# Optimization experiments

Hardware: AMD Instinct MI355X
Metric: run time of the kernel (lower is better)

Reference implementation:

```python
import jax, jax.numpy as jnp
import numpy as np

B, T, I, H, O = 64, 512, 256, 1024, 10

def setup_inputs() -> dict:
    key = jax.random.key(0)
    ks = jax.random.split(key, 7)
    s_x = 1.0 / np.sqrt(I)
    s_h = 1.0 / np.sqrt(H)
    return {
        "x": jax.random.normal(ks[0], (B, T, I), dtype=jnp.float32),
        "Wx": jax.random.uniform(ks[1], (4, I, H), jnp.float32, -s_x, s_x),
        "bx": jax.random.uniform(ks[2], (4, H), jnp.float32, -s_x, s_x),
        "Wh": jax.random.uniform(ks[3], (4, H, H), jnp.float32, -s_h, s_h),
        "bh": jax.random.uniform(ks[4], (4, H), jnp.float32, -s_h, s_h),
        "Wp": jax.random.uniform(ks[5], (H, O), jnp.float32, -s_h, s_h),
        "bp": jax.random.uniform(ks[6], (O,), jnp.float32, -s_h, s_h),
    }

def reference(x, Wx, bx, Wh, bh, Wp, bp):
    # Gate order along axis 0: g (tanh), i, f, o (sigmoid).
    batch, seq, _ = x.shape
    hid = Wh.shape[-1]
    # Precompute all input-side gate projections: [T, 4, B, H]
    gx_all = jnp.einsum('bti,kih->tkbh', x, Wx) + bx[None, :, None, :]

    def step(carry, gx_t):
        h, c = carry
        z = gx_t + jnp.einsum('bh,kho->kbo', h, Wh) + bh[:, None, :]  # [4,B,H]
        g = jnp.tanh(z[0])
        i = jax.nn.sigmoid(z[1])
        f = jax.nn.sigmoid(z[2])
        o = jax.nn.sigmoid(z[3])
        c = g * i + c * f
        h = jnp.tanh(c) * o
        return (h, c), None

    h0 = jnp.zeros((batch, hid), dtype=x.dtype)
    c0 = jnp.zeros((batch, hid), dtype=x.dtype)
    (h, _), _ = jax.lax.scan(step, (h0, c0), gx_all)
    p = h @ Wp + bp
    return jax.nn.softmax(p, axis=1)
```

## Files before the change

### kernel.cpp

```cpp
#include <hip/hip_runtime.h>
#include <cstdint>
#include <cstddef>

#define B_  64
#define T_  512
#define I_  256
#define H_  1024
#define O_  10
#define ZST 68
#define ZPW (64 * ZST)
#define ZBUF (4 * ZPW)
#define LDS_ALLOC 139264

typedef __attribute__((ext_vector_type(4))) float f32x4;
typedef __attribute__((ext_vector_type(8))) short s16x8;
typedef unsigned long long u64;

__device__ inline unsigned short f2bf(float f) {
    unsigned int u = __float_as_uint(f);
    u += 0x7fffu + ((u >> 16) & 1u);
    return (unsigned short)(u >> 16);
}
__device__ inline float bf2f(unsigned short h) {
    return __uint_as_float(((unsigned int)h) << 16);
}
__device__ inline float fsig(float x)  { return 1.0f / (1.0f + __expf(-x)); }
__device__ inline float ftanh(float x) { return 1.0f - 2.0f / (1.0f + __expf(2.0f * x)); }

#define ALD32(p)    __hip_atomic_load((p), __ATOMIC_RELAXED, __HIP_MEMORY_SCOPE_AGENT)
#define AST32(p, v) __hip_atomic_store((p), (v), __ATOMIC_RELAXED, __HIP_MEMORY_SCOPE_AGENT)
#define ALD64(p)    __hip_atomic_load((p), __ATOMIC_RELAXED, __HIP_MEMORY_SCOPE_AGENT)
#define AST64(p, v) __hip_atomic_store((p), (v), __ATOMIC_RELAXED, __HIP_MEMORY_SCOPE_AGENT)

#define PIN_A(x) asm volatile("" : "+a"(x))

__global__ __launch_bounds__(256) void cast_xT_kernel(const float* __restrict__ x,
                                                      unsigned short* __restrict__ xb) {
    int idx = blockIdx.x * 256 + threadIdx.x;
    int ic4 = idx & 63, rest = idx >> 6;
    int t = rest & 511, b = rest >> 9;
    float4 v = ((const float4*)x)[((size_t)(b * T_ + t)) * 64 + ic4];
    ((ushort4*)xb)[((size_t)(t * B_ + b)) * 64 + ic4] =
        make_ushort4(f2bf(v.x), f2bf(v.y), f2bf(v.z), f2bf(v.w));
}

__global__ __launch_bounds__(256) void pack_wh_kernel(const float* __restrict__ Wh,
                                                      uint4* __restrict__ whp) {
    int e = blockIdx.x * 256 + threadIdx.x;
    int lane = e & 63, nt = (e >> 6) & 3, kt = (e >> 8) & 31, nb = e >> 13;
    int q = (lane & 15) >> 2, cc = lane & 3;
    int hh = nb * 16 + nt * 4 + cc;
    int k0 = kt * 32 + (lane >> 4) * 8;
    const float* src = Wh + (size_t)q * (H_ * H_) + (size_t)k0 * H_ + hh;
    unsigned short u[8];
#pragma unroll
    for (int j = 0; j < 8; ++j) u[j] = f2bf(src[(size_t)j * H_]);
    uint4 out;
    out.x = (unsigned)u[0] | ((unsigned)u[1] << 16);
    out.y = (unsigned)u[2] | ((unsigned)u[3] << 16);
    out.z = (unsigned)u[4] | ((unsigned)u[5] << 16);
    out.w = (unsigned)u[6] | ((unsigned)u[7] << 16);
    whp[e] = out;
}

__global__ __launch_bounds__(256) void pack_wx_kernel(const float* __restrict__ Wx,
                                                      uint4* __restrict__ wxp) {
    int e = blockIdx.x * 256 + threadIdx.x;
    int lane = e & 63, nt = (e >> 6) & 3, kt = (e >> 8) & 7, nb = e >> 11;
    int q = (lane & 15) >> 2, cc = lane & 3;
    int hh = nb * 16 + nt * 4 + cc;
    int i0 = kt * 32 + (lane >> 4) * 8;
    const float* src = Wx + (size_t)q * (I_ * H_) + (size_t)i0 * H_ + hh;
    unsigned short u[8];
#pragma unroll
    for (int j = 0; j < 8; ++j) u[j] = f2bf(src[(size_t)j * H_]);
    uint4 out;
    out.x = (unsigned)u[0] | ((unsigned)u[1] << 16);
    out.y = (unsigned)u[2] | ((unsigned)u[3] << 16);
    out.z = (unsigned)u[4] | ((unsigned)u[5] << 16);
    out.w = (unsigned)u[6] | ((unsigned)u[7] << 16);
    wxp[e] = out;
}

__global__ __launch_bounds__(256, 1) void lstm_kernel(const unsigned short* __restrict__ xb,
                                                      const uint4* __restrict__ whp,
                                                      const uint4* __restrict__ wxp,
                                                      const float* __restrict__ bx,
                                                      const float* __restrict__ bh,
                                                      const float* __restrict__ Wp,
                                                      const float* __restrict__ bp,
                                                      unsigned short* __restrict__ hbuf,
                                                      unsigned int* __restrict__ flags,
                                                      float* __restrict__ out) {
    extern __shared__ float zpart[];
    int tid = threadIdx.x, lane = tid & 63, w = tid >> 6;
    int nb = blockIdx.x;
    unsigned int* done = flags + 768;

    if (nb >= 64) {
        float a = 1.0f + (float)tid * 0.001f;
        const float bm = 1.0000001f, cm = 0.9999999f;
        while (ALD32(done) == 0u) {
#pragma unroll
            for (int i = 0; i < 512; ++i) a = __builtin_fmaf(a, bm, cm);
        }
        if (__float_as_uint(a) == 0xDEADBEEFu) AST32(&flags[200], 1u);
        return;
    }

    int ma = lane & 15, quad = lane >> 4;

    const s16x8* whpp = (const s16x8*)whp;
    const s16x8* wxpp = (const s16x8*)wxp;
    s16x8 whf[4][8], wxf[4][2];
#pragma unroll
    for (int nt = 0; nt < 4; ++nt) {
#pragma unroll
        for (int k = 0; k < 8; ++k)
            whf[nt][k] = whpp[nb * 8192 + (w * 8 + k) * 256 + nt * 64 + lane];
#pragma unroll
        for (int k = 0; k < 2; ++k)
            wxf[nt][k] = wxpp[nb * 2048 + (w * 2 + k) * 256 + nt * 64 + lane];
    }
#pragma unroll
    for (int nt = 0; nt < 4; ++nt) {
#pragma unroll
        for (int k = 0; k < 8; ++k) PIN_A(whf[nt][k]);
#pragma unroll
        for (int k = 0; k < 2; ++k) PIN_A(wxf[nt][k]);
    }

    int gb = tid >> 2, wq = tid & 3;
    float bias[4][4];
#pragma unroll
    for (int g = 0; g < 4; ++g)
#pragma unroll
        for (int i = 0; i < 4; ++i) {
            int n = g * H_ + nb * 16 + wq * 4 + i;
            bias[g][i] = bx[n] + bh[n];
        }

    u64* hbase = (u64*)hbuf;

    AST64(&hbase[nb * 256 + tid], 0ull);
    asm volatile("s_waitcnt vmcnt(0)" ::: "memory");
    if (lane == 0) AST32(&flags[nb * 4 + w], 1u);

    float cst[4] = {0.f, 0.f, 0.f, 0.f};

    for (int t = 0; t < T_; ++t) {
        s16x8 Ax[4][2];
#pragma unroll
        for (int mt = 0; mt < 4; ++mt) {
            const unsigned short* xrow =
                xb + ((size_t)t * B_ + mt * 16 + ma) * I_ + w * 64 + quad * 8;
            Ax[mt][0] = *(const s16x8*)xrow;
            Ax[mt][1] = *(const s16x8*)(xrow + 32);
        }
        unsigned probe = ALD32(&flags[w * 64 + lane]);
        __builtin_amdgcn_sched_barrier(0);

        f32x4 acc[4][4] = {};
#pragma unroll
        for (int mt = 0; mt < 4; ++mt)
#pragma unroll
            for (int kx = 0; kx < 2; ++kx)
#pragma unroll
                for (int nt = 0; nt < 4; ++nt)
                    acc[mt][nt] = __builtin_amdgcn_mfma_f32_16x16x32_bf16(Ax[mt][kx], wxf[nt][kx],
                                                                          acc[mt][nt], 0, 0, 0);
        __builtin_amdgcn_sched_barrier(0);

        {
            unsigned tgt = (unsigned)(t + 1);
            if (__ballot(probe < tgt) != 0ull) {
                for (;;) {
                    unsigned v = ALD32(&flags[w * 64 + lane]);
                    if (__ballot(v < tgt) == 0ull) break;
                    __builtin_amdgcn_s_sleep(1);
                }
            }
        }

        const u64* hp = hbase + (size_t)(t & 3) * 16384;
        u64*       hn = hbase + (size_t)((t + 1) & 3) * 16384;

        u64 Ah[4][16];
#pragma unroll
        for (int mt = 0; mt < 4; ++mt) {
            int row = mt * 16 + ma;
#pragma unroll
            for (int kl = 0; kl < 8; ++kl) {
                const u64* p = hp + ((size_t)((w * 8 + kl) * 2 + (quad >> 1))) * 256
                               + (size_t)row * 4 + (quad & 1) * 2;
                Ah[mt][kl * 2]     = ALD64(p);
                Ah[mt][kl * 2 + 1] = ALD64(p + 1);
            }
        }

#pragma unroll
        for (int mt = 0; mt < 4; ++mt) {
#pragma unroll
            for (int kl = 0; kl < 8; ++kl) {
                union { u64 q[2]; s16x8 v; } au;
                au.q[0] = Ah[mt][kl * 2];
                au.q[1] = Ah[mt][kl * 2 + 1];
#pragma unroll
                for (int nt = 0; nt < 4; ++nt)
                    acc[mt][nt] = __builtin_amdgcn_mfma_f32_16x16x32_bf16(au.v, whf[nt][kl],
                                                                          acc[mt][nt], 0, 0, 0);
            }
        }

        float* zb = zpart + (size_t)(t & 1) * ZBUF;
        float* zp = zb + w * ZPW;
#pragma unroll
        for (int mt = 0; mt < 4; ++mt)
#pragma unroll
            for (int nt = 0; nt < 4; ++nt)
#pragma unroll
                for (int r = 0; r < 4; ++r)
                    zp[(mt * 16 + quad * 4 + r) * ZST + nt * 16 + ma] = acc[mt][nt][r];
        __syncthreads();

        float zs[4][4];
#pragma unroll
        for (int g = 0; g < 4; ++g) {
            float4 s = make_float4(0.f, 0.f, 0.f, 0.f);
#pragma unroll
            for (int p = 0; p < 4; ++p) {
                float4 v = *(const float4*)(zb + p * ZPW + gb * ZST + wq * 16 + g * 4);
                s.x += v.x; s.y += v.y; s.z += v.z; s.w += v.w;
            }
            zs[g][0] = s.x; zs[g][1] = s.y; zs[g][2] = s.z; zs[g][3] = s.w;
        }
        unsigned short hh[4];
#pragma unroll
        for (int i = 0; i < 4; ++i) {
            float g  = ftanh(zs[0][i] + bias[0][i]);
            float ii = fsig (zs[1][i] + bias[1][i]);
            float ff = fsig (zs[2][i] + bias[2][i]);
            float oo = fsig (zs[3][i] + bias[3][i]);
            float c  = g * ii + cst[i] * ff;
            cst[i] = c;
            hh[i] = f2bf(ftanh(c) * oo);
        }
        u64 hv = (u64)hh[0] | ((u64)hh[1] << 16) | ((u64)hh[2] << 32) | ((u64)hh[3] << 48);
        AST64(&hn[nb * 256 + tid], hv);

        asm volatile("s_waitcnt vmcnt(0)" ::: "memory");
        if (lane == 0) AST32(&flags[nb * 4 + w], (unsigned)(t + 2));
    }

    {
        unsigned tgt = (unsigned)(T_ + 1);
        for (;;) {
            unsigned v = ALD32(&flags[w * 64 + lane]);
            if (__ballot(v < tgt) == 0ull) break;
            __builtin_amdgcn_s_sleep(1);
        }
    }
    __syncthreads();
    if (nb == 0 && tid == 0) AST32(done, 1u);

    int b = nb;
    union { u64 q; unsigned short s[4]; } hu;
    hu.q = ALD64(&hbase[(tid >> 2) * 256 + b * 4 + (tid & 3)]);
    int j0 = (tid >> 2) * 16 + (tid & 3) * 4;
    float pacc[O_];
#pragma unroll
    for (int o = 0; o < O_; ++o) pacc[o] = 0.f;
#pragma unroll
    for (int j = 0; j < 4; ++j) {
        float hvv = bf2f(hu.s[j]);
        const float* wr = Wp + (size_t)(j0 + j) * O_;
#pragma unroll
        for (int o = 0; o < O_; ++o) pacc[o] += hvv * wr[o];
    }
    float* red = zpart;
#pragma unroll
    for (int o = 0; o < O_; ++o) red[tid * O_ + o] = pacc[o];
    __syncthreads();
    for (int s2 = 128; s2 > 0; s2 >>= 1) {
        if (tid < s2) {
#pragma unroll
            for (int o = 0; o < O_; ++o) red[tid * O_ + o] += red[(tid + s2) * O_ + o];
        }
        __syncthreads();
    }
    if (tid == 0) {
        float p[O_];
        for (int o = 0; o < O_; ++o) p[o] = red[o] + bp[o];
        float mx = p[0];
        for (int o = 1; o < O_; ++o) mx = fmaxf(mx, p[o]);
        float e[O_], sum = 0.f;
        for (int o = 0; o < O_; ++o) { e[o] = __expf(p[o] - mx); sum += e[o]; }
        float inv = 1.f / sum;
        for (int o = 0; o < O_; ++o) out[b * O_ + o] = e[o] * inv;
    }
}

extern "C" void kernel_launch(void* const* d_in, const int* in_sizes, int n_in,
                              void* d_out, int out_size, void* d_ws, size_t ws_size,
                              hipStream_t stream) {
    (void)in_sizes; (void)n_in; (void)out_size; (void)ws_size;
    const float* x  = (const float*)d_in[0];
    const float* Wx = (const float*)d_in[1];
    const float* bx = (const float*)d_in[2];
    const float* Wh = (const float*)d_in[3];
    const float* bh = (const float*)d_in[4];
    const float* Wp = (const float*)d_in[5];
    const float* bp = (const float*)d_in[6];

    const size_t xbB  = (size_t)T_ * B_ * I_ * 2;
    const size_t whpB = (size_t)4 * H_ * H_ * 2;
    const size_t wxpB = (size_t)4 * I_ * H_ * 2;
    const size_t hB   = (size_t)4 * B_ * H_ * 2;

    char* ws = (char*)d_ws;
    unsigned short* xb    = (unsigned short*)ws;
    uint4*          whp   = (uint4*)(ws + xbB);
    uint4*          wxp   = (uint4*)(ws + xbB + whpB);
    unsigned short* hbuf  = (unsigned short*)(ws + xbB + whpB + wxpB);
    unsigned int*   flags = (unsigned int*)(ws + xbB + whpB + wxpB + hB);

    static bool attr_set = false;
    if (!attr_set) {
        (void)hipFuncSetAttribute((const void*)lstm_kernel,
                                  hipFuncAttributeMaxDynamicSharedMemorySize, LDS_ALLOC);
        attr_set = true;
    }

    hipError_t e0 = hipMemsetAsync(flags, 0, 4096, stream);
    (void)e0;
    cast_xT_kernel<<<8192, 256, 0, stream>>>(x, xb);
    pack_wh_kernel<<<2048, 256, 0, stream>>>(Wh, whp);
    pack_wx_kernel<<< 512, 256, 0, stream>>>(Wx, wxp);
    lstm_kernel<<<64 + 192, 256, LDS_ALLOC, stream>>>(xb, whp, wxp, bx, bh, Wp, bp, hbuf, flags,
                                                      (float*)d_out);
}
```

Baseline: 3.726 ms.

## Replace per-step flag barrier with NaN-sentinel polling on hidden state buffer

Removes the per-timestep flag publish and flag spin-wait between workgroups. Consumers now read the h buffer directly and re-poll any 64-bit chunk that still holds a bf16 NaN sentinel. Producers reset the slot two steps ahead to the sentinel, and a new kernel pre-fills the 4-slot ring. This drops a vmcnt drain and a flag round trip from the critical path each step. The cost is repeated polling of many h words, and correctness now relies on no real h value equalling the sentinel and on ordering of the relaxed stores.

Result: slower. 5.015 ms (+34.6%).

```diff
diff --git a/kernel.cpp b/kernel.cpp
--- a/kernel.cpp
+++ b/kernel.cpp
@@ -16,6 +16,8 @@
 typedef __attribute__((ext_vector_type(8))) short s16x8;
 typedef unsigned long long u64;
 
+#define SENT 0x7FC07FC07FC07FC0ull
+
 __device__ inline unsigned short f2bf(float f) {
     unsigned int u = __float_as_uint(f);
     u += 0x7fffu + ((u >> 16) & 1u);
@@ -80,6 +82,11 @@
     out.z = (unsigned)u[4] | ((unsigned)u[5] << 16);
     out.w = (unsigned)u[6] | ((unsigned)u[7] << 16);
     wxp[e] = out;
+}
+
+__global__ __launch_bounds__(256) void fill_sent_kernel(u64* __restrict__ hb) {
+    int i = blockIdx.x * 256 + threadIdx.x;
+    hb[i] = SENT;
 }
 
 __global__ __launch_bounds__(256, 1) void lstm_kernel(const unsigned short* __restrict__ xb,
@@ -143,8 +150,6 @@
     u64* hbase = (u64*)hbuf;
 
     AST64(&hbase[nb * 256 + tid], 0ull);
-    asm volatile("s_waitcnt vmcnt(0)" ::: "memory");
-    if (lane == 0) AST32(&flags[nb * 4 + w], 1u);
 
     float cst[4] = {0.f, 0.f, 0.f, 0.f};
 
@@ -156,30 +161,6 @@
                 xb + ((size_t)t * B_ + mt * 16 + ma) * I_ + w * 64 + quad * 8;
             Ax[mt][0] = *(const s16x8*)xrow;
             Ax[mt][1] = *(const s16x8*)(xrow + 32);
-        }
-        unsigned probe = ALD32(&flags[w * 64 + lane]);
-        __builtin_amdgcn_sched_barrier(0);
-
-        f32x4 acc[4][4] = {};
-#pragma unroll
-        for (int mt = 0; mt < 4; ++mt)
-#pragma unroll
-            for (int kx = 0; kx < 2; ++kx)
-#pragma unroll
-                for (int nt = 0; nt < 4; ++nt)
-                    acc[mt][nt] = __builtin_amdgcn_mfma_f32_16x16x32_bf16(Ax[mt][kx], wxf[nt][kx],
-                                                                          acc[mt][nt], 0, 0, 0);
-        __builtin_amdgcn_sched_barrier(0);
-
-        {
-            unsigned tgt = (unsigned)(t + 1);
-            if (__ballot(probe < tgt) != 0ull) {
-                for (;;) {
-                    unsigned v = ALD32(&flags[w * 64 + lane]);
-                    if (__ballot(v < tgt) == 0ull) break;
-                    __builtin_amdgcn_s_sleep(1);
-                }
-            }
         }
 
         const u64* hp = hbase + (size_t)(t & 3) * 16384;
@@ -197,6 +178,51 @@
                 Ah[mt][kl * 2 + 1] = ALD64(p + 1);
             }
         }
+        __builtin_amdgcn_sched_barrier(0);
+
+        f32x4 acc[4][4] = {};
+#pragma unroll
+        for (int mt = 0; mt < 4; ++mt)
+#pragma unroll
+            for (int nt = 0; nt < 4; ++nt) PIN_A(acc[mt][nt]);
+#pragma unroll
+        for (int mt = 0; mt < 4; ++mt)
+#pragma unroll
+            for (int kx = 0; kx < 2; ++kx)
+#pragma unroll
+                for (int nt = 0; nt < 4; ++nt)
+                    acc[mt][nt] = __builtin_amdgcn_mfma_f32_16x16x32_bf16(Ax[mt][kx], wxf[nt][kx],
+                                                                          acc[mt][nt], 0, 0, 0);
+        __builtin_amdgcn_sched_barrier(0);
+
+        {
+            bool any = false;
+#pragma unroll
+            for (int mt = 0; mt < 4; ++mt)
+#pragma unroll
+                for (int k = 0; k < 16; ++k) any |= (Ah[mt][k] == SENT);
+            while (__ballot(any) != 0ull) {
+                __builtin_amdgcn_s_sleep(1);
+#pragma unroll
+                for (int mt = 0; mt < 4; ++mt) {
+                    int row = mt * 16 + ma;
+#pragma unroll
+                    for (int kl = 0; kl < 8; ++kl) {
+                        if (Ah[mt][kl * 2] == SENT || Ah[mt][kl * 2 + 1] == SENT) {
+                            const u64* p = hp + ((size_t)((w * 8 + kl) * 2 + (quad >> 1))) * 256
+                                           + (size_t)row * 4 + (quad & 1) * 2;
+                            Ah[mt][kl * 2]     = ALD64(p);
+                            Ah[mt][kl * 2 + 1] = ALD64(p + 1);
+                        }
+                    }
+                }
+                any = false;
+#pragma unroll
+                for (int mt = 0; mt < 4; ++mt)
+#pragma unroll
+                    for (int k = 0; k < 16; ++k) any |= (Ah[mt][k] == SENT);
+            }
+        }
 
 #pragma unroll
         for (int mt = 0; mt < 4; ++mt) {
@@ -210,6 +236,11 @@
                     acc[mt][nt] = __builtin_amdgcn_mfma_f32_16x16x32_bf16(au.v, whf[nt][kl],
                                                                           acc[mt][nt], 0, 0, 0);
             }
+        }
+
+        {
+            u64* hf = hbase + (size_t)((t + 2) & 3) * 16384;
+            AST64(&hf[nb * 256 + tid], SENT);
         }
 
         float* zb = zpart + (size_t)(t & 1) * ZBUF;
@@ -247,11 +278,10 @@
         }
         u64 hv = (u64)hh[0] | ((u64)hh[1] << 16) | ((u64)hh[2] << 32) | ((u64)hh[3] << 48);
         AST64(&hn[nb * 256 + tid], hv);
-
-        asm volatile("s_waitcnt vmcnt(0)" ::: "memory");
-        if (lane == 0) AST32(&flags[nb * 4 + w], (unsigned)(t + 2));
-    }
-
+    }
+
+    asm volatile("s_waitcnt vmcnt(0)" ::: "memory");
+    if (lane == 0) AST32(&flags[nb * 4 + w], (unsigned)(T_ + 1));
     {
         unsigned tgt = (unsigned)(T_ + 1);
         for (;;) {
@@ -336,6 +366,7 @@
     cast_xT_kernel<<<8192, 256, 0, stream>>>(x, xb);
     pack_wh_kernel<<<2048, 256, 0, stream>>>(Wh, whp);
     pack_wx_kernel<<< 512, 256, 0, stream>>>(Wx, wxp);
+    fill_sent_kernel<<<256, 256, 0, stream>>>((u64*)hbuf);
     lstm_kernel<<<64 + 192, 256, LDS_ALLOC, stream>>>(xb, whp, wxp, bx, bh, Wp, bp, hbuf, flags,
                                                       (float*)d_out);
 }
```
